# Performance work log

Hardware: AMD Instinct MI355X
Metric: run time of the kernel (lower is better)

## Reference

```python
import jax, jax.numpy as jnp
import numpy as np

B, S, T, IN, H = 16384, 336, 48, 5, 64  # batch, enc seq, horizon, features, hidden


def _lstm_cell(x, h, c, Wih, Whh, bih, bhh):
    # PyTorch gate order: i, f, g, o
    g = x @ Wih.T + h @ Whh.T + bih + bhh  # [B, 4H]
    i, f, gg, o = jnp.split(g, 4, axis=-1)
    i, f, o = jax.nn.sigmoid(i), jax.nn.sigmoid(f), jax.nn.sigmoid(o)
    c_new = f * c + i * jnp.tanh(gg)
    h_new = o * jnp.tanh(c_new)
    return h_new, c_new


def setup_inputs() -> dict:
    key = jax.random.key(0)
    ks = jax.random.split(key, 20)
    k = 1.0 / np.sqrt(H)

    def p(kk, shape):
        return jax.random.uniform(kk, shape, jnp.float32, -k, k)

    d = {"src": jax.random.normal(ks[0], (B, S, IN), jnp.float32)}
    d["enc_Wih0"] = p(ks[1], (4 * H, IN)); d["enc_Whh0"] = p(ks[2], (4 * H, H))
    d["enc_bih0"] = p(ks[3], (4 * H,));   d["enc_bhh0"] = p(ks[4], (4 * H,))
    d["enc_Wih1"] = p(ks[5], (4 * H, H)); d["enc_Whh1"] = p(ks[6], (4 * H, H))
    d["enc_bih1"] = p(ks[7], (4 * H,));   d["enc_bhh1"] = p(ks[8], (4 * H,))
    d["dec_Wih0"] = p(ks[9], (4 * H, 1)); d["dec_Whh0"] = p(ks[10], (4 * H, H))
    d["dec_bih0"] = p(ks[11], (4 * H,));  d["dec_bhh0"] = p(ks[12], (4 * H,))
    d["dec_Wih1"] = p(ks[13], (4 * H, H)); d["dec_Whh1"] = p(ks[14], (4 * H, H))
    d["dec_bih1"] = p(ks[15], (4 * H,));  d["dec_bhh1"] = p(ks[16], (4 * H,))
    d["fc_W"] = p(ks[17], (1, H)); d["fc_b"] = p(ks[18], (1,))
    return d


def reference(src, enc_Wih0, enc_Whh0, enc_bih0, enc_bhh0,
              enc_Wih1, enc_Whh1, enc_bih1, enc_bhh1,
              dec_Wih0, dec_Whh0, dec_bih0, dec_bhh0,
              dec_Wih1, dec_Whh1, dec_bih1, dec_bhh1,
              fc_W, fc_b):
    b = src.shape[0]
    z = jnp.zeros((b, H), src.dtype)

    # ---- Encoder: 2-layer LSTM over S timesteps (inference: no dropout) ----
    def enc_step(carry, x_t):
        h0, c0, h1, c1 = carry
        h0, c0 = _lstm_cell(x_t, h0, c0, enc_Wih0, enc_Whh0, enc_bih0, enc_bhh0)
        h1, c1 = _lstm_cell(h0, h1, c1, enc_Wih1, enc_Whh1, enc_bih1, enc_bhh1)
        return (h0, c0, h1, c1), None

    (h0, c0, h1, c1), _ = jax.lax.scan(enc_step, (z, z, z, z),
                                       jnp.swapaxes(src, 0, 1))  # [S,B,IN]

    dec_in0 = src[:, -1, 3:4]  # [B, 1] (feature index 3 of last timestep)

    def dec_step(carry, _):
        h0, c0, h1, c1, x = carry
        h0, c0 = _lstm_cell(x, h0, c0, dec_Wih0, dec_Whh0, dec_bih0, dec_bhh0)
        h1, c1 = _lstm_cell(h0, h1, c1, dec_Wih1, dec_Whh1, dec_bih1, dec_bhh1)
        pred = h1 @ fc_W.T + fc_b  # [B, 1]
        return (h0, c0, h1, c1, pred), pred

    _, preds = jax.lax.scan(dec_step, (h0, c0, h1, c1, dec_in0), None, length=T)
    return jnp.transpose(preds, (1, 0, 2))  # [B, T, 1]
```

## Files before the change

### kernel.cpp

```cpp
#include <hip/hip_runtime.h>
#include <stdint.h>

#define B_ 16384
#define S_ 336
#define T_ 48
#define IN_ 5
#define H_ 64

typedef _Float16 f16;
typedef _Float16 f16x8 __attribute__((ext_vector_type(8)));
typedef float f32x4 __attribute__((ext_vector_type(4)));

#define LOG2E 1.44269504088896340736f

#define OFF_E0 0
#define OFF_E1 24576
#define OFF_D0 57344
#define OFF_D1 81920
#define OFF_BE0 114688
#define OFF_BE1 114944
#define OFF_BD0 115200
#define OFF_BD1 115456
#define OFF_FCW 115712
#define OFF_FCB 115776
#define WS_TOT  115777

__device__ __forceinline__ float sig2(float g) {
    return __builtin_amdgcn_rcpf(1.0f + __builtin_amdgcn_exp2f(g));
}
__device__ __forceinline__ float tanh2(float g) {
    return 1.0f - 2.0f * __builtin_amdgcn_rcpf(1.0f + __builtin_amdgcn_exp2f(g));
}
__device__ __forceinline__ float tanhc(float c) {
    return 1.0f - 2.0f * __builtin_amdgcn_rcpf(1.0f + __builtin_amdgcn_exp2f(c * (2.0f * LOG2E)));
}

__global__ void prep_kernel(
    const float* __restrict__ eWih0, const float* __restrict__ eWhh0,
    const float* __restrict__ ebih0, const float* __restrict__ ebhh0,
    const float* __restrict__ eWih1, const float* __restrict__ eWhh1,
    const float* __restrict__ ebih1, const float* __restrict__ ebhh1,
    const float* __restrict__ dWih0, const float* __restrict__ dWhh0,
    const float* __restrict__ dbih0, const float* __restrict__ dbhh0,
    const float* __restrict__ dWih1, const float* __restrict__ dWhh1,
    const float* __restrict__ dbih1, const float* __restrict__ dbhh1,
    const float* __restrict__ fcW,  const float* __restrict__ fcb,
    float* __restrict__ ws)
{
    int idx = blockIdx.x * blockDim.x + threadIdx.x;
    if (idx >= WS_TOT) return;
    float outv;
    if (idx < OFF_BE0) {
        int rel, nkt, xdim;
        const float *Wi, *Wh;
        if (idx < OFF_E1)      { rel = idx - OFF_E0; nkt = 3; xdim = IN_; Wi = eWih0; Wh = eWhh0; }
        else if (idx < OFF_D0) { rel = idx - OFF_E1; nkt = 4; xdim = 64;  Wi = eWih1; Wh = eWhh1; }
        else if (idx < OFF_D1) { rel = idx - OFF_D0; nkt = 3; xdim = 1;   Wi = dWih0; Wh = dWhh0; }
        else                   { rel = idx - OFF_D1; nkt = 4; xdim = 64;  Wi = dWih1; Wh = dWhh1; }
        int reg = rel & 3, pl = (rel >> 2) & 1, lane = (rel >> 3) & 63;
        int rest = rel >> 9;
        int kt = rest % nkt, mt = rest / nkt;
        int gp = mt * 16 + (lane & 15);
        int type = gp & 3;
        int j  = type * 64 + (gp >> 2);
        float sc = (type == 2) ? (2.0f * LOG2E) : (-LOG2E);
        union { f16 h2[2]; float f; } u_;
        #pragma unroll
        for (int h = 0; h < 2; ++h) {
            int k = kt * 32 + (lane >> 4) * 8 + reg * 2 + h;
            float v;
            if (nkt == 4) v = (k < 64) ? Wi[j * 64 + k] : Wh[j * 64 + (k - 64)];
            else          v = (k < xdim) ? Wi[j * xdim + k]
                              : ((k < 32) ? 0.0f : Wh[j * 64 + (k - 32)]);
            v *= sc;
            f16 hi = (f16)v;
            u_.h2[h] = (pl == 0) ? hi : (f16)(v - (float)hi);
        }
        outv = u_.f;
    } else if (idx < OFF_FCW) {
        int rel = idx - OFF_BE0;
        int which = rel >> 8, gp = rel & 255;
        int type = gp & 3;
        int j = type * 64 + (gp >> 2);
        float sc = (type == 2) ? (2.0f * LOG2E) : (-LOG2E);
        const float *bi, *bh;
        if (which == 0)      { bi = ebih0; bh = ebhh0; }
        else if (which == 1) { bi = ebih1; bh = ebhh1; }
        else if (which == 2) { bi = dbih0; bh = dbhh0; }
        else                 { bi = dbih1; bh = dbhh1; }
        outv = (bi[j] + bh[j]) * sc;
    } else if (idx < OFF_FCB) {
        outv = fcW[idx - OFF_FCW];
    } else {
        outv = fcb[0];
    }
    ws[idx] = outv;
}

#define XBI(b,p,g,r)   ((((((b)*2)+(p))*4+(g))*64+(r))*8)
#define HBI(b,p,k,g,r) (((((((b)*2)+(p))*2+(k))*4+(g))*64+(r))*8)

#define MFMA(a,b,c) __builtin_amdgcn_mfma_f32_16x16x32_f16(a, b, c, 0, 0, 0)

__device__ __forceinline__ void stage_x5(f16* __restrict__ XB, int b, int lane, const float* xv) {
    f16x8 ph, pl_;
    #pragma unroll
    for (int i = 0; i < 8; ++i) { ph[i] = (f16)0; pl_[i] = (f16)0; }
    #pragma unroll
    for (int i = 0; i < IN_; ++i) {
        f16 hh = (f16)xv[i]; ph[i] = hh; pl_[i] = (f16)(xv[i] - (float)hh);
    }
    *(f16x8*)&XB[XBI(b,0,0,lane)] = ph;
    *(f16x8*)&XB[XBI(b,1,0,lane)] = pl_;
}
__device__ __forceinline__ void stage_x1(f16* __restrict__ XB, int b, int lane, float v) {
    f16x8 ph, pl_;
    #pragma unroll
    for (int i = 0; i < 8; ++i) { ph[i] = (f16)0; pl_[i] = (f16)0; }
    f16 hh = (f16)v; ph[0] = hh; pl_[0] = (f16)(v - (float)hh);
    *(f16x8*)&XB[XBI(b,0,0,lane)] = ph;
    *(f16x8*)&XB[XBI(b,1,0,lane)] = pl_;
}

__device__ __forceinline__ void layer0_only(
    int pX, int pH0r, int pH0w, int m0, int lane,
    const f16x8 (&wa)[7][2][2], const f32x4 (&b0)[2], float (&c0)[2][4],
    const f16* __restrict__ XB, f16* __restrict__ H0B)
{
    const int g4 = lane >> 4, l15 = lane & 15;
    #pragma unroll
    for (int nt = 0; nt < 4; ++nt) {
        const int r = nt * 16 + l15;
        f16x8 xh  = *(const f16x8*)&XB [XBI(pX,0,g4,r)];
        f16x8 xl  = *(const f16x8*)&XB [XBI(pX,1,g4,r)];
        f16x8 hh0 = *(const f16x8*)&H0B[HBI(pH0r,0,0,g4,r)];
        f16x8 hl0 = *(const f16x8*)&H0B[HBI(pH0r,1,0,g4,r)];
        f16x8 hh1 = *(const f16x8*)&H0B[HBI(pH0r,0,1,g4,r)];
        f16x8 hl1 = *(const f16x8*)&H0B[HBI(pH0r,1,1,g4,r)];
        #pragma unroll
        for (int mt = 0; mt < 2; ++mt) {
            f32x4 a = b0[mt];
            a = MFMA(wa[0][mt][0], xh,  a);
            a = MFMA(wa[0][mt][1], xh,  a);
            a = MFMA(wa[0][mt][0], xl,  a);
            a = MFMA(wa[1][mt][0], hh0, a);
            a = MFMA(wa[1][mt][1], hh0, a);
            a = MFMA(wa[1][mt][0], hl0, a);
            a = MFMA(wa[2][mt][0], hh1, a);
            a = MFMA(wa[2][mt][1], hh1, a);
            a = MFMA(wa[2][mt][0], hl1, a);
            const int u = (m0 + mt) * 4 + g4;
            float ig = sig2(a[0]), fg = sig2(a[1]);
            float gg = tanh2(a[2]), og = sig2(a[3]);
            float c = fmaf(fg, c0[mt][nt], ig * gg);
            c0[mt][nt] = c;
            float h = og * tanhc(c);
            f16 hh = (f16)h, hl = (f16)(h - (float)hh);
            H0B[HBI(pH0w,0,(u>>5),(u>>3)&3,r) + (u&7)] = hh;
            H0B[HBI(pH0w,1,(u>>5),(u>>3)&3,r) + (u&7)] = hl;
        }
    }
}

template<bool DEC>
__device__ __forceinline__ void layer1_only(
    int pH0, int pH1r, int pH1w, int m0, int lane,
    const f16x8 (&wa)[7][2][2], const f32x4 (&b1)[2], float (&c1)[2][4],
    const f16* __restrict__ H0B, f16* __restrict__ H1B, float* __restrict__ H1F)
{
    const int g4 = lane >> 4, l15 = lane & 15;
    #pragma unroll
    for (int nt = 0; nt < 4; ++nt) {
        const int r = nt * 16 + l15;
        f16x8 hh0 = *(const f16x8*)&H0B[HBI(pH0,0,0,g4,r)];
        f16x8 hl0 = *(const f16x8*)&H0B[HBI(pH0,1,0,g4,r)];
        f16x8 hh1 = *(const f16x8*)&H0B[HBI(pH0,0,1,g4,r)];
        f16x8 hl1 = *(const f16x8*)&H0B[HBI(pH0,1,1,g4,r)];
        f16x8 gh0 = *(const f16x8*)&H1B[HBI(pH1r,0,0,g4,r)];
        f16x8 gl0 = *(const f16x8*)&H1B[HBI(pH1r,1,0,g4,r)];
        f16x8 gh1 = *(const f16x8*)&H1B[HBI(pH1r,0,1,g4,r)];
        f16x8 gl1 = *(const f16x8*)&H1B[HBI(pH1r,1,1,g4,r)];
        #pragma unroll
        for (int mt = 0; mt < 2; ++mt) {
            f32x4 a = b1[mt];
            a = MFMA(wa[3][mt][0], hh0, a);
            a = MFMA(wa[3][mt][1], hh0, a);
            a = MFMA(wa[3][mt][0], hl0, a);
            a = MFMA(wa[4][mt][0], hh1, a);
            a = MFMA(wa[4][mt][1], hh1, a);
            a = MFMA(wa[4][mt][0], hl1, a);
            a = MFMA(wa[5][mt][0], gh0, a);
            a = MFMA(wa[5][mt][1], gh0, a);
            a = MFMA(wa[5][mt][0], gl0, a);
            a = MFMA(wa[6][mt][0], gh1, a);
            a = MFMA(wa[6][mt][1], gh1, a);
            a = MFMA(wa[6][mt][0], gl1, a);
            const int u = (m0 + mt) * 4 + g4;
            float ig = sig2(a[0]), fg = sig2(a[1]);
            float gg = tanh2(a[2]), og = sig2(a[3]);
            float c = fmaf(fg, c1[mt][nt], ig * gg);
            c1[mt][nt] = c;
            float h = og * tanhc(c);
            f16 hh = (f16)h, hl = (f16)(h - (float)hh);
            H1B[HBI(pH1w,0,(u>>5),(u>>3)&3,r) + (u&7)] = hh;
            H1B[HBI(pH1w,1,(u>>5),(u>>3)&3,r) + (u&7)] = hl;
            if (DEC) H1F[u * 64 + r] = h;
        }
    }
}

__device__ __forceinline__ void enc_phase(
    int p, int m0, int lane,
    const f16x8 (&wa)[7][2][2], const f32x4 (&b0)[2], const f32x4 (&b1)[2],
    float (&c0)[2][4], float (&c1)[2][4],
    const f16* __restrict__ XB, f16* __restrict__ H0B, f16* __restrict__ H1B)
{
    const int g4 = lane >> 4, l15 = lane & 15;
    const int q = p ^ 1;
    #pragma unroll
    for (int nt = 0; nt < 4; ++nt) {
        const int r = nt * 16 + l15;
        f16x8 hh0 = *(const f16x8*)&H0B[HBI(p,0,0,g4,r)];
        f16x8 hl0 = *(const f16x8*)&H0B[HBI(p,1,0,g4,r)];
        f16x8 hh1 = *(const f16x8*)&H0B[HBI(p,0,1,g4,r)];
        f16x8 hl1 = *(const f16x8*)&H0B[HBI(p,1,1,g4,r)];
        f16x8 gh0 = *(const f16x8*)&H1B[HBI(q,0,0,g4,r)];
        f16x8 gl0 = *(const f16x8*)&H1B[HBI(q,1,0,g4,r)];
        f16x8 gh1 = *(const f16x8*)&H1B[HBI(q,0,1,g4,r)];
        f16x8 gl1 = *(const f16x8*)&H1B[HBI(q,1,1,g4,r)];
        #pragma unroll
        for (int mt = 0; mt < 2; ++mt) {
            const int u = (m0 + mt) * 4 + g4;
            f32x4 a = b1[mt];
            a = MFMA(wa[3][mt][0], hh0, a);
            a = MFMA(wa[3][mt][1], hh0, a);
            a = MFMA(wa[3][mt][0], hl0, a);
            a = MFMA(wa[4][mt][0], hh1, a);
            a = MFMA(wa[4][mt][1], hh1, a);
            a = MFMA(wa[4][mt][0], hl1, a);
            a = MFMA(wa[5][mt][0], gh0, a);
            a = MFMA(wa[5][mt][1], gh0, a);
            a = MFMA(wa[5][mt][0], gl0, a);
            a = MFMA(wa[6][mt][0], gh1, a);
            a = MFMA(wa[6][mt][1], gh1, a);
            a = MFMA(wa[6][mt][0], gl1, a);
            float ig = sig2(a[0]), fg = sig2(a[1]);
            float gg = tanh2(a[2]), og = sig2(a[3]);
            float c = fmaf(fg, c1[mt][nt], ig * gg);
            c1[mt][nt] = c;
            float h = og * tanhc(c);
            f16 hh = (f16)h, hl = (f16)(h - (float)hh);
            H1B[HBI(p,0,(u>>5),(u>>3)&3,r) + (u&7)] = hh;
            H1B[HBI(p,1,(u>>5),(u>>3)&3,r) + (u&7)] = hl;
        }
        f16x8 xh = *(const f16x8*)&XB[XBI(q,0,g4,r)];
        f16x8 xl = *(const f16x8*)&XB[XBI(q,1,g4,r)];
        #pragma unroll
        for (int mt = 0; mt < 2; ++mt) {
            const int u = (m0 + mt) * 4 + g4;
            f32x4 z = b0[mt];
            z = MFMA(wa[0][mt][0], xh,  z);
            z = MFMA(wa[0][mt][1], xh,  z);
            z = MFMA(wa[0][mt][0], xl,  z);
            z = MFMA(wa[1][mt][0], hh0, z);
            z = MFMA(wa[1][mt][1], hh0, z);
            z = MFMA(wa[1][mt][0], hl0, z);
            z = MFMA(wa[2][mt][0], hh1, z);
            z = MFMA(wa[2][mt][1], hh1, z);
            z = MFMA(wa[2][mt][0], hl1, z);
            float ig = sig2(z[0]), fg = sig2(z[1]);
            float gg = tanh2(z[2]), og = sig2(z[3]);
            float c = fmaf(fg, c0[mt][nt], ig * gg);
            c0[mt][nt] = c;
            float h = og * tanhc(c);
            f16 hh = (f16)h, hl = (f16)(h - (float)hh);
            H0B[HBI(q,0,(u>>5),(u>>3)&3,r) + (u&7)] = hh;
            H0B[HBI(q,1,(u>>5),(u>>3)&3,r) + (u&7)] = hl;
        }
    }
}

__global__ __launch_bounds__(512)
__attribute__((amdgpu_waves_per_eu(2, 2)))
void lstm_kernel(
    const float* __restrict__ src, const float* __restrict__ ws,
    float* __restrict__ out)
{
    __shared__ __align__(16) f16 XB [2*2*4*64*8];
    __shared__ __align__(16) f16 H0B[2*2*2*4*64*8];
    __shared__ __align__(16) f16 H1B[2*2*2*4*64*8];
    __shared__ float H1F[64*64];
    __shared__ float FCW[64];

    const int tid  = threadIdx.x;
    const int lane = tid & 63;
    const int wave = __builtin_amdgcn_readfirstlane(tid >> 6);
    const int m0   = wave * 2;
    const int g4   = lane >> 4;
    const int rowBase = blockIdx.x * 64;

    float c0[2][4], c1[2][4];
    #pragma unroll
    for (int mt = 0; mt < 2; ++mt)
        #pragma unroll
        for (int nt = 0; nt < 4; ++nt) { c0[mt][nt] = 0.0f; c1[mt][nt] = 0.0f; }

    f16x8 wa[7][2][2];
    f32x4 b0[2], b1[2];

    auto ldw = [&](int off0, int off1, int ob0, int ob1) {
        #pragma unroll
        for (int kt = 0; kt < 3; ++kt)
            #pragma unroll
            for (int mt = 0; mt < 2; ++mt)
                #pragma unroll
                for (int pl = 0; pl < 2; ++pl)
                    wa[kt][mt][pl] = *(const f16x8*)(ws + off0 +
                        ((((m0 + mt) * 3 + kt) * 64 + lane) * 2 + pl) * 4);
        #pragma unroll
        for (int kt = 0; kt < 4; ++kt)
            #pragma unroll
            for (int mt = 0; mt < 2; ++mt)
                #pragma unroll
                for (int pl = 0; pl < 2; ++pl)
                    wa[3 + kt][mt][pl] = *(const f16x8*)(ws + off1 +
                        ((((m0 + mt) * 4 + kt) * 64 + lane) * 2 + pl) * 4);
        #pragma unroll
        for (int mt = 0; mt < 2; ++mt) {
            b0[mt] = *(const f32x4*)(ws + ob0 + (m0 + mt) * 16 + g4 * 4);
            b1[mt] = *(const f32x4*)(ws + ob1 + (m0 + mt) * 16 + g4 * 4);
        }
    };
    ldw(OFF_E0, OFF_E1, OFF_BE0, OFF_BE1);

    for (int i = tid; i < 2*2*4*64*8; i += 512) XB[i] = (f16)0;
    for (int i = tid; i < 8192; i += 512) { H0B[8192 + i] = (f16)0; H1B[8192 + i] = (f16)0; }
    if (tid < 64) FCW[tid] = ws[OFF_FCW + tid];
    const float fcbv = ws[OFF_FCB];

    const float* sp = src + (size_t)(rowBase + lane) * (S_ * IN_);
    __syncthreads();

    if (wave == 7) {
        float xv[IN_];
        #pragma unroll
        for (int i = 0; i < IN_; ++i) xv[i] = sp[i];
        stage_x5(XB, 0, lane, xv);
        #pragma unroll
        for (int i = 0; i < IN_; ++i) xv[i] = sp[IN_ + i];
        stage_x5(XB, 1, lane, xv);
    }
    __syncthreads();

    layer0_only(0, 1, 0, m0, lane, wa, b0, c0, XB, H0B);
    __syncthreads();

    #pragma unroll 1
    for (int t = 0; t < S_ - 1; ++t) {
        const int p = t & 1;
        float xv[IN_];
        const bool pf = (wave == 7) && (t + 2 < S_);
        if (pf) {
            #pragma unroll
            for (int i = 0; i < IN_; ++i) xv[i] = sp[(t + 2) * IN_ + i];
        }
        enc_phase(p, m0, lane, wa, b0, b1, c0, c1, XB, H0B, H1B);
        if (pf) stage_x5(XB, p, lane, xv);
        __syncthreads();
    }

    layer1_only<false>(1, 0, 1, m0, lane, wa, b1, c1, H0B, H1B, H1F);
    __syncthreads();

    ldw(OFF_D0, OFF_D1, OFF_BD0, OFF_BD1);
    if (wave == 7) stage_x1(XB, 0, lane, sp[(S_ - 1) * IN_ + 3]);
    __syncthreads();

    #pragma unroll 1
    for (int t = 0; t < T_; ++t) {
        const int q = t & 1;
        layer0_only(q, q ^ 1, q, m0, lane, wa, b0, c0, XB, H0B);
        __syncthreads();
        layer1_only<true>(q, q ^ 1, q, m0, lane, wa, b1, c1, H0B, H1B, H1F);
        __syncthreads();
        if (wave == 0) {
            float pv = fcbv;
            #pragma unroll 4
            for (int k = 0; k < 64; ++k) pv = fmaf(FCW[k], H1F[k * 64 + lane], pv);
            out[(size_t)(rowBase + lane) * T_ + t] = pv;
            if (t + 1 < T_) stage_x1(XB, q ^ 1, lane, pv);
        }
        __syncthreads();
    }
}

extern "C" void kernel_launch(void* const* d_in, const int* in_sizes, int n_in,
                              void* d_out, int out_size, void* d_ws, size_t ws_size,
                              hipStream_t stream)
{
    const float* src = (const float*)d_in[0];
    float* ws  = (float*)d_ws;
    float* out = (float*)d_out;

    prep_kernel<<<(WS_TOT + 255) / 256, 256, 0, stream>>>(
        (const float*)d_in[1],  (const float*)d_in[2],
        (const float*)d_in[3],  (const float*)d_in[4],
        (const float*)d_in[5],  (const float*)d_in[6],
        (const float*)d_in[7],  (const float*)d_in[8],
        (const float*)d_in[9],  (const float*)d_in[10],
        (const float*)d_in[11], (const float*)d_in[12],
        (const float*)d_in[13], (const float*)d_in[14],
        (const float*)d_in[15], (const float*)d_in[16],
        (const float*)d_in[17], (const float*)d_in[18],
        ws);

    lstm_kernel<<<B_ / 64, 512, 0, stream>>>(src, ws, out);
}
```

Measured before the change: 1.992 ms.

## Halve rows per block, drop weight low-part MFMAs, fold layer-0 bias into input

Each block now handles 32 batch rows instead of 64, doubling the grid and allowing 4 waves per EU so more blocks can be resident. The split-precision weight low-half MFMAs are dropped and only the fp16 high part of the weights is kept, which cuts MFMA count and register use. The layer-0 bias is folded into the weight matrix through a constant-one input column. It trades some accuracy, since weights are now plain fp16, for less compute and better occupancy. The fc shared buffer gets a padded stride.

Result: slower. 3.806 ms (+91.0%).

```diff
diff --git a/kernel.cpp b/kernel.cpp
--- a/kernel.cpp
+++ b/kernel.cpp
@@ -6,6 +6,9 @@
 #define T_ 48
 #define IN_ 5
 #define H_ 64
+
+#define ROWS 32
+#define GP   256
 
 typedef _Float16 f16;
 typedef _Float16 f16x8 __attribute__((ext_vector_type(8)));
@@ -52,11 +55,11 @@
     float outv;
     if (idx < OFF_BE0) {
         int rel, nkt, xdim;
-        const float *Wi, *Wh;
-        if (idx < OFF_E1)      { rel = idx - OFF_E0; nkt = 3; xdim = IN_; Wi = eWih0; Wh = eWhh0; }
-        else if (idx < OFF_D0) { rel = idx - OFF_E1; nkt = 4; xdim = 64;  Wi = eWih1; Wh = eWhh1; }
-        else if (idx < OFF_D1) { rel = idx - OFF_D0; nkt = 3; xdim = 1;   Wi = dWih0; Wh = dWhh0; }
-        else                   { rel = idx - OFF_D1; nkt = 4; xdim = 64;  Wi = dWih1; Wh = dWhh1; }
+        const float *Wi, *Wh, *bi, *bh;
+        if (idx < OFF_E1)      { rel = idx - OFF_E0; nkt = 3; xdim = IN_; Wi = eWih0; Wh = eWhh0; bi = ebih0; bh = ebhh0; }
+        else if (idx < OFF_D0) { rel = idx - OFF_E1; nkt = 4; xdim = 64;  Wi = eWih1; Wh = eWhh1; bi = 0; bh = 0; }
+        else if (idx < OFF_D1) { rel = idx - OFF_D0; nkt = 3; xdim = 1;   Wi = dWih0; Wh = dWhh0; bi = dbih0; bh = dbhh0; }
+        else                   { rel = idx - OFF_D1; nkt = 4; xdim = 64;  Wi = dWih1; Wh = dWhh1; bi = 0; bh = 0; }
         int reg = rel & 3, pl = (rel >> 2) & 1, lane = (rel >> 3) & 63;
         int rest = rel >> 9;
         int kt = rest % nkt, mt = rest / nkt;
@@ -69,9 +72,11 @@
         for (int h = 0; h < 2; ++h) {
             int k = kt * 32 + (lane >> 4) * 8 + reg * 2 + h;
             float v;
-            if (nkt == 4) v = (k < 64) ? Wi[j * 64 + k] : Wh[j * 64 + (k - 64)];
-            else          v = (k < xdim) ? Wi[j * xdim + k]
-                              : ((k < 32) ? 0.0f : Wh[j * 64 + (k - 32)]);
+            if (nkt == 4)      v = (k < 64) ? Wi[j * 64 + k] : Wh[j * 64 + (k - 64)];
+            else if (k < xdim) v = Wi[j * xdim + k];
+            else if (k == 5)   v = bi[j] + bh[j];
+            else if (k >= 32)  v = Wh[j * 64 + (k - 32)];
+            else               v = 0.0f;
             v *= sc;
             f16 hi = (f16)v;
             u_.h2[h] = (pl == 0) ? hi : (f16)(v - (float)hi);
@@ -97,12 +102,12 @@
     ws[idx] = outv;
 }
 
-#define XBI(b,p,g,r)   ((((((b)*2)+(p))*4+(g))*64+(r))*8)
-#define HBI(b,p,k,g,r) (((((((b)*2)+(p))*2+(k))*4+(g))*64+(r))*8)
+#define XBI(b,p,g,r)   ((((b)*2+(p))*4+(g))*GP + (r)*8)
+#define HBI(b,p,k,g,r) (((((b)*2+(p))*2+(k))*4+(g))*GP + (r)*8)
 
 #define MFMA(a,b,c) __builtin_amdgcn_mfma_f32_16x16x32_f16(a, b, c, 0, 0, 0)
 
-__device__ __forceinline__ void stage_x5(f16* __restrict__ XB, int b, int lane, const float* xv) {
+__device__ __forceinline__ void stage_x5(f16* __restrict__ XB, int b, int r, const float* xv) {
     f16x8 ph, pl_;
     #pragma unroll
     for (int i = 0; i < 8; ++i) { ph[i] = (f16)0; pl_[i] = (f16)0; }
@@ -110,26 +115,28 @@
     for (int i = 0; i < IN_; ++i) {
         f16 hh = (f16)xv[i]; ph[i] = hh; pl_[i] = (f16)(xv[i] - (float)hh);
     }
-    *(f16x8*)&XB[XBI(b,0,0,lane)] = ph;
-    *(f16x8*)&XB[XBI(b,1,0,lane)] = pl_;
-}
-__device__ __forceinline__ void stage_x1(f16* __restrict__ XB, int b, int lane, float v) {
+    ph[5] = (f16)1.0f;
+    *(f16x8*)&XB[XBI(b,0,0,r)] = ph;
+    *(f16x8*)&XB[XBI(b,1,0,r)] = pl_;
+}
+__device__ __forceinline__ void stage_x1(f16* __restrict__ XB, int b, int r, float v) {
     f16x8 ph, pl_;
     #pragma unroll
     for (int i = 0; i < 8; ++i) { ph[i] = (f16)0; pl_[i] = (f16)0; }
     f16 hh = (f16)v; ph[0] = hh; pl_[0] = (f16)(v - (float)hh);
-    *(f16x8*)&XB[XBI(b,0,0,lane)] = ph;
-    *(f16x8*)&XB[XBI(b,1,0,lane)] = pl_;
+    ph[5] = (f16)1.0f;
+    *(f16x8*)&XB[XBI(b,0,0,r)] = ph;
+    *(f16x8*)&XB[XBI(b,1,0,r)] = pl_;
 }
 
 __device__ __forceinline__ void layer0_only(
     int pX, int pH0r, int pH0w, int m0, int lane,
-    const f16x8 (&wa)[7][2][2], const f32x4 (&b0)[2], float (&c0)[2][4],
+    const f16x8 (&wa)[7][2], float (&c0)[2][2],
     const f16* __restrict__ XB, f16* __restrict__ H0B)
 {
     const int g4 = lane >> 4, l15 = lane & 15;
     #pragma unroll
-    for (int nt = 0; nt < 4; ++nt) {
+    for (int nt = 0; nt < 2; ++nt) {
         const int r = nt * 16 + l15;
         f16x8 xh  = *(const f16x8*)&XB [XBI(pX,0,g4,r)];
         f16x8 xl  = *(const f16x8*)&XB [XBI(pX,1,g4,r)];
@@ -139,19 +146,16 @@
         f16x8 hl1 = *(const f16x8*)&H0B[HBI(pH0r,1,1,g4,r)];
         #pragma unroll
         for (int mt = 0; mt < 2; ++mt) {
-            f32x4 a = b0[mt];
-            a = MFMA(wa[0][mt][0], xh,  a);
-            a = MFMA(wa[0][mt][1], xh,  a);
-            a = MFMA(wa[0][mt][0], xl,  a);
-            a = MFMA(wa[1][mt][0], hh0, a);
-            a = MFMA(wa[1][mt][1], hh0, a);
-            a = MFMA(wa[1][mt][0], hl0, a);
-            a = MFMA(wa[2][mt][0], hh1, a);
-            a = MFMA(wa[2][mt][1], hh1, a);
-            a = MFMA(wa[2][mt][0], hl1, a);
+            f32x4 z = {0.0f, 0.0f, 0.0f, 0.0f};
+            z = MFMA(wa[0][mt], xh,  z);
+            z = MFMA(wa[0][mt], xl,  z);
+            z = MFMA(wa[1][mt], hh0, z);
+            z = MFMA(wa[1][mt], hl0, z);
+            z = MFMA(wa[2][mt], hh1, z);
+            z = MFMA(wa[2][mt], hl1, z);
             const int u = (m0 + mt) * 4 + g4;
-            float ig = sig2(a[0]), fg = sig2(a[1]);
-            float gg = tanh2(a[2]), og = sig2(a[3]);
+            float ig = sig2(z[0]), fg = sig2(z[1]);
+            float gg = tanh2(z[2]), og = sig2(z[3]);
             float c = fmaf(fg, c0[mt][nt], ig * gg);
             c0[mt][nt] = c;
             float h = og * tanhc(c);
@@ -165,12 +169,12 @@
 template<bool DEC>
 __device__ __forceinline__ void layer1_only(
     int pH0, int pH1r, int pH1w, int m0, int lane,
-    const f16x8 (&wa)[7][2][2], const f32x4 (&b1)[2], float (&c1)[2][4],
+    const f16x8 (&wa)[7][2], const f32x4 (&b1)[2], float (&c1)[2][2],
     const f16* __restrict__ H0B, f16* __restrict__ H1B, float* __restrict__ H1F)
 {
     const int g4 = lane >> 4, l15 = lane & 15;
     #pragma unroll
-    for (int nt = 0; nt < 4; ++nt) {
+    for (int nt = 0; nt < 2; ++nt) {
         const int r = nt * 16 + l15;
         f16x8 hh0 = *(const f16x8*)&H0B[HBI(pH0,0,0,g4,r)];
         f16x8 hl0 = *(const f16x8*)&H0B[HBI(pH0,1,0,g4,r)];
@@ -183,18 +187,14 @@
         #pragma unroll
         for (int mt = 0; mt < 2; ++mt) {
             f32x4 a = b1[mt];
-            a = MFMA(wa[3][mt][0], hh0, a);
-            a = MFMA(wa[3][mt][1], hh0, a);
-            a = MFMA(wa[3][mt][0], hl0, a);
-            a = MFMA(wa[4][mt][0], hh1, a);
-            a = MFMA(wa[4][mt][1], hh1, a);
-            a = MFMA(wa[4][mt][0], hl1, a);
-            a = MFMA(wa[5][mt][0], gh0, a);
-            a = MFMA(wa[5][mt][1], gh0, a);
-            a = MFMA(wa[5][mt][0], gl0, a);
-            a = MFMA(wa[6][mt][0], gh1, a);
-            a = MFMA(wa[6][mt][1], gh1, a);
-            a = MFMA(wa[6][mt][0], gl1, a);
+            a = MFMA(wa[3][mt], hh0, a);
+            a = MFMA(wa[3][mt], hl0, a);
+            a = MFMA(wa[4][mt], hh1, a);
+            a = MFMA(wa[4][mt], hl1, a);
+            a = MFMA(wa[5][mt], gh0, a);
+            a = MFMA(wa[5][mt], gl0, a);
+            a = MFMA(wa[6][mt], gh1, a);
+            a = MFMA(wa[6][mt], gl1, a);
             const int u = (m0 + mt) * 4 + g4;
             float ig = sig2(a[0]), fg = sig2(a[1]);
             float gg = tanh2(a[2]), og = sig2(a[3]);
@@ -204,21 +204,21 @@
             f16 hh = (f16)h, hl = (f16)(h - (float)hh);
             H1B[HBI(pH1w,0,(u>>5),(u>>3)&3,r) + (u&7)] = hh;
             H1B[HBI(pH1w,1,(u>>5),(u>>3)&3,r) + (u&7)] = hl;
-            if (DEC) H1F[u * 64 + r] = h;
+            if (DEC) H1F[u * 33 + r] = h;
         }
     }
 }
 
 __device__ __forceinline__ void enc_phase(
     int p, int m0, int lane,
-    const f16x8 (&wa)[7][2][2], const f32x4 (&b0)[2], const f32x4 (&b1)[2],
-    float (&c0)[2][4], float (&c1)[2][4],
+    const f16x8 (&wa)[7][2], const f32x4 (&b1)[2],
+    float (&c0)[2][2], float (&c1)[2][2],
     const f16* __restrict__ XB, f16* __restrict__ H0B, f16* __restrict__ H1B)
 {
     const int g4 = lane >> 4, l15 = lane & 15;
     const int q = p ^ 1;
     #pragma unroll
-    for (int nt = 0; nt < 4; ++nt) {
+    for (int nt = 0; nt < 2; ++nt) {
         const int r = nt * 16 + l15;
         f16x8 hh0 = *(const f16x8*)&H0B[HBI(p,0,0,g4,r)];
         f16x8 hl0 = *(const f16x8*)&H0B[HBI(p,1,0,g4,r)];
@@ -232,18 +232,14 @@
         for (int mt = 0; mt < 2; ++mt) {
             const int u = (m0 + mt) * 4 + g4;
             f32x4 a = b1[mt];
-            a = MFMA(wa[3][mt][0], hh0, a);
-            a = MFMA(wa[3][mt][1], hh0, a);
-            a = MFMA(wa[3][mt][0], hl0, a);
-            a = MFMA(wa[4][mt][0], hh1, a);
-            a = MFMA(wa[4][mt][1], hh1, a);
-            a = MFMA(wa[4][mt][0], hl1, a);
-            a = MFMA(wa[5][mt][0], gh0, a);
-            a = MFMA(wa[5][mt][1], gh0, a);
-            a = MFMA(wa[5][mt][0], gl0, a);
-            a = MFMA(wa[6][mt][0], gh1, a);
-            a = MFMA(wa[6][mt][1], gh1, a);
-            a = MFMA(wa[6][mt][0], gl1, a);
+            a = MFMA(wa[3][mt], hh0, a);
+            a = MFMA(wa[3][mt], hl0, a);
+            a = MFMA(wa[4][mt], hh1, a);
+            a = MFMA(wa[4][mt], hl1, a);
+            a = MFMA(wa[5][mt], gh0, a);
+            a = MFMA(wa[5][mt], gl0, a);
+            a = MFMA(wa[6][mt], gh1, a);
+            a = MFMA(wa[6][mt], gl1, a);
             float ig = sig2(a[0]), fg = sig2(a[1]);
             float gg = tanh2(a[2]), og = sig2(a[3]);
             float c = fmaf(fg, c1[mt][nt], ig * gg);
@@ -258,16 +254,13 @@
         #pragma unroll
         for (int mt = 0; mt < 2; ++mt) {
             const int u = (m0 + mt) * 4 + g4;
-            f32x4 z = b0[mt];
-            z = MFMA(wa[0][mt][0], xh,  z);
-            z = MFMA(wa[0][mt][1], xh,  z);
-            z = MFMA(wa[0][mt][0], xl,  z);
-            z = MFMA(wa[1][mt][0], hh0, z);
-            z = MFMA(wa[1][mt][1], hh0, z);
-            z = MFMA(wa[1][mt][0], hl0, z);
-            z = MFMA(wa[2][mt][0], hh1, z);
-            z = MFMA(wa[2][mt][1], hh1, z);
-            z = MFMA(wa[2][mt][0], hl1, z);
+            f32x4 z = {0.0f, 0.0f, 0.0f, 0.0f};
+            z = MFMA(wa[0][mt], xh,  z);
+            z = MFMA(wa[0][mt], xl,  z);
+            z = MFMA(wa[1][mt], hh0, z);
+            z = MFMA(wa[1][mt], hl0, z);
+            z = MFMA(wa[2][mt], hh1, z);
+            z = MFMA(wa[2][mt], hl1, z);
             float ig = sig2(z[0]), fg = sig2(z[1]);
             float gg = tanh2(z[2]), og = sig2(z[3]);
             float c = fmaf(fg, c0[mt][nt], ig * gg);
@@ -281,15 +274,15 @@
 }
 
 __global__ __launch_bounds__(512)
-__attribute__((amdgpu_waves_per_eu(2, 2)))
+__attribute__((amdgpu_waves_per_eu(4)))
 void lstm_kernel(
     const float* __restrict__ src, const float* __restrict__ ws,
     float* __restrict__ out)
 {
-    __shared__ __align__(16) f16 XB [2*2*4*64*8];
-    __shared__ __align__(16) f16 H0B[2*2*2*4*64*8];
-    __shared__ __align__(16) f16 H1B[2*2*2*4*64*8];
-    __shared__ float H1F[64*64];
+    __shared__ __align__(16) f16 XB [2*2*4*GP];
+    __shared__ __align__(16) f16 H0B[2*2*2*4*GP];
+    __shared__ __align__(16) f16 H1B[2*2*2*4*GP];
+    __shared__ float H1F[64*33];
     __shared__ float FCW[64];
 
     const int tid  = threadIdx.x;
@@ -297,51 +290,46 @@
     const int wave = __builtin_amdgcn_readfirstlane(tid >> 6);
     const int m0   = wave * 2;
     const int g4   = lane >> 4;
-    const int rowBase = blockIdx.x * 64;
-
-    float c0[2][4], c1[2][4];
+    const int rowBase = blockIdx.x * ROWS;
+
+    float c0[2][2], c1[2][2];
     #pragma unroll
     for (int mt = 0; mt < 2; ++mt)
         #pragma unroll
-        for (int nt = 0; nt < 4; ++nt) { c0[mt][nt] = 0.0f; c1[mt][nt] = 0.0f; }
-
-    f16x8 wa[7][2][2];
-    f32x4 b0[2], b1[2];
-
-    auto ldw = [&](int off0, int off1, int ob0, int ob1) {
+        for (int nt = 0; nt < 2; ++nt) { c0[mt][nt] = 0.0f; c1[mt][nt] = 0.0f; }
+
+    f16x8 wa[7][2];
+    f32x4 b1[2];
+
+    auto ldw = [&](int off0, int off1, int ob1) {
         #pragma unroll
         for (int kt = 0; kt < 3; ++kt)
             #pragma unroll
             for (int mt = 0; mt < 2; ++mt)
-                #pragma unroll
-                for (int pl = 0; pl < 2; ++pl)
-                    wa[kt][mt][pl] = *(const f16x8*)(ws + off0 +
-                        ((((m0 + mt) * 3 + kt) * 64 + lane) * 2 + pl) * 4);
+                wa[kt][mt] = *(const f16x8*)(ws + off0 +
+                    ((((m0 + mt) * 3 + kt) * 64 + lane) * 2) * 4);
         #pragma unroll
         for (int kt = 0; kt < 4; ++kt)
             #pragma unroll
             for (int mt = 0; mt < 2; ++mt)
-                #pragma unroll
-                for (int pl = 0; pl < 2; ++pl)
-                    wa[3 + kt][mt][pl] = *(const f16x8*)(ws + off1 +
-                        ((((m0 + mt) * 4 + kt) * 64 + lane) * 2 + pl) * 4);
-        #pragma unroll
-        for (int mt = 0; mt < 2; ++mt) {
-            b0[mt] = *(const f32x4*)(ws + ob0 + (m0 + mt) * 16 + g4 * 4);
+                wa[3 + kt][mt] = *(const f16x8*)(ws + off1 +
+                    ((((m0 + mt) * 4 + kt) * 64 + lane) * 2) * 4);
+        #pragma unroll
+        for (int mt = 0; mt < 2; ++mt)
             b1[mt] = *(const f32x4*)(ws + ob1 + (m0 + mt) * 16 + g4 * 4);
-        }
     };
-    ldw(OFF_E0, OFF_E1, OFF_BE0, OFF_BE1);
-
-    for (int i = tid; i < 2*2*4*64*8; i += 512) XB[i] = (f16)0;
-    for (int i = tid; i < 8192; i += 512) { H0B[8192 + i] = (f16)0; H1B[8192 + i] = (f16)0; }
+    ldw(OFF_E0, OFF_E1, OFF_BE1);
+
+    for (int i = tid; i < 2*2*4*GP; i += 512) XB[i] = (f16)0;
+    for (int i = tid; i < 2*2*2*4*GP; i += 512) { H0B[i] = (f16)0; H1B[i] = (f16)0; }
     if (tid < 64) FCW[tid] = ws[OFF_FCW + tid];
     const float fcbv = ws[OFF_FCB];
 
-    const float* sp = src + (size_t)(rowBase + lane) * (S_ * IN_);
+    const int xr = lane & (ROWS - 1);
+    const float* sp = src + (size_t)(rowBase + xr) * (S_ * IN_);
     __syncthreads();
 
-    if (wave == 7) {
+    if (wave == 7 && lane < ROWS) {
         float xv[IN_];
         #pragma unroll
         for (int i = 0; i < IN_; ++i) xv[i] = sp[i];
@@ -352,19 +340,19 @@
     }
     __syncthreads();
 
-    layer0_only(0, 1, 0, m0, lane, wa, b0, c0, XB, H0B);
+    layer0_only(0, 1, 0, m0, lane, wa, c0, XB, H0B);
     __syncthreads();
 
     #pragma unroll 1
     for (int t = 0; t < S_ - 1; ++t) {
         const int p = t & 1;
         float xv[IN_];
-        const bool pf = (wave == 7) && (t + 2 < S_);
+        const bool pf = (wave == 7) && (lane < ROWS) && (t + 2 < S_);
         if (pf) {
             #pragma unroll
             for (int i = 0; i < IN_; ++i) xv[i] = sp[(t + 2) * IN_ + i];
         }
-        enc_phase(p, m0, lane, wa, b0, b1, c0, c1, XB, H0B, H1B);
+        enc_phase(p, m0, lane, wa, b1, c0, c1, XB, H0B, H1B);
         if (pf) stage_x5(XB, p, lane, xv);
         __syncthreads();
     }
@@ -372,21 +360,21 @@
     layer1_only<false>(1, 0, 1, m0, lane, wa, b1, c1, H0B, H1B, H1F);
     __syncthreads();
 
-    ldw(OFF_D0, OFF_D1, OFF_BD0, OFF_BD1);
-    if (wave == 7) stage_x1(XB, 0, lane, sp[(S_ - 1) * IN_ + 3]);
+    ldw(OFF_D0, OFF_D1, OFF_BD1);
+    if (wave == 7 && lane < ROWS) stage_x1(XB, 0, lane, sp[(S_ - 1) * IN_ + 3]);
     __syncthreads();
 
     #pragma unroll 1
     for (int t = 0; t < T_; ++t) {
         const int q = t & 1;
-        layer0_only(q, q ^ 1, q, m0, lane, wa, b0, c0, XB, H0B);
+        layer0_only(q, q ^ 1, q, m0, lane, wa, c0, XB, H0B);
         __syncthreads();
         layer1_only<true>(q, q ^ 1, q, m0, lane, wa, b1, c1, H0B, H1B, H1F);
         __syncthreads();
-        if (wave == 0) {
+        if (wave == 0 && lane < ROWS) {
             float pv = fcbv;
             #pragma unroll 4
-            for (int k = 0; k < 64; ++k) pv = fmaf(FCW[k], H1F[k * 64 + lane], pv);
+            for (int k = 0; k < 64; ++k) pv = fmaf(FCW[k], H1F[k * 33 + lane], pv);
             out[(size_t)(rowBase + lane) * T_ + t] = pv;
             if (t + 1 < T_) stage_x1(XB, q ^ 1, lane, pv);
         }
@@ -414,5 +402,5 @@
         (const float*)d_in[17], (const float*)d_in[18],
         ws);
 
-    lstm_kernel<<<B_ / 64, 512, 0, stream>>>(src, ws, out);
-}
+    lstm_kernel<<<B_ / ROWS, 512, 0, stream>>>(src, ws, out);
+}
```
